# Performance work log

Measured on AMD Instinct MI355X. Metric: run time of the kernel, lower is better.

The kernel has to match this reference:

```python
import jax, jax.numpy as jnp
import numpy as np

B, S, I, H = 1024, 200, 4, 128  # batch, seq_len, interest_num, hidden_size
ROUTING_TIMES = 3
EPS = 1e-9


def setup_inputs() -> dict:
    key = jax.random.key(0)
    k1, k2, k3 = jax.random.split(key, 3)
    item_eb = jax.random.normal(k1, (B, S, H), dtype=jnp.float32)
    mask = jax.random.randint(k2, (B, S), 0, 2, dtype=jnp.int32)
    w = jax.random.normal(k3, (1, S, I * H, H), dtype=jnp.float32)
    return {"item_eb": item_eb, "mask": mask, "w": w}


def _squash_factor(cap):
    # cap: [B, I, 1, H]; standard capsule squash scale
    n = jnp.sum(jnp.square(cap), axis=-1, keepdims=True)
    return n / (1.0 + n) / jnp.sqrt(n + EPS)


def reference(item_eb, mask, w):
    # bilinear_type == 2: item_eb_hat[b,s,i] = sum_h w[0,s,i,h] * item_eb[b,s,h]
    hat = jnp.einsum('bsh,sjh->bsj', item_eb, w[0])          # [B, S, I*H]
    hat = hat.reshape(B, S, I, H).transpose(0, 2, 1, 3)      # [B, I, S, H]
    hat_iter = jax.lax.stop_gradient(hat)                    # stop_grad=True

    atten_mask = mask[:, None, :]                            # [B, 1, S] broadcasts over I
    capsule_weight = jnp.zeros((B, I, S), dtype=item_eb.dtype)

    interest_capsule = None
    for i in range(ROUTING_TIMES):
        sw = jax.nn.softmax(capsule_weight, axis=-1)         # [B, I, S]
        sw = jnp.where(atten_mask == 0, jnp.zeros_like(sw), sw)
        sw = sw[:, :, None, :]                               # [B, I, 1, S]
        src = hat_iter if i < ROUTING_TIMES - 1 else hat
        interest_capsule = jnp.matmul(sw, src)               # [B, I, 1, H]
        interest_capsule = _squash_factor(interest_capsule) * interest_capsule
        if i < ROUTING_TIMES - 1:
            # delta[b,i,s] = <hat_iter[b,i,s,:], capsule[b,i,0,:]>
            delta = jnp.matmul(hat_iter, jnp.swapaxes(interest_capsule, 2, 3))
            capsule_weight = capsule_weight + delta.reshape(B, I, S)

    return interest_capsule.reshape(B, I, H)
```

## Files before the change

### kernel.cpp

```cpp
#include <hip/hip_runtime.h>
#include <hip/hip_bf16.h>
#include <cstdint>

#define SDIM 200
#define HDIM 128
#define IDIM 4
#define BDIM 1024
#define LDK 72
#define LDEF 132

typedef __attribute__((ext_vector_type(8))) short short8;
typedef __attribute__((ext_vector_type(4))) float f32x4;

__device__ __forceinline__ ushort f32_to_bf16u(float f) {
    uint32_t u = __builtin_bit_cast(uint32_t, f);
    u += 0x7FFFu + ((u >> 16) & 1u);
    return (ushort)(u >> 16);
}
__device__ __forceinline__ float bf16u_to_f32(ushort h) {
    uint32_t u = ((uint32_t)h) << 16;
    return __builtin_bit_cast(float, u);
}
__device__ __forceinline__ void split8(const float* p, uint4* hi, uint4* lo) {
    union { ushort u[8]; uint4 v; } xh, xl;
    #pragma unroll
    for (int j = 0; j < 8; ++j) {
        float f = p[j];
        ushort h = f32_to_bf16u(f);
        float r = f - bf16u_to_f32(h);
        xh.u[j] = h;
        xl.u[j] = f32_to_bf16u(r);
    }
    *hi = xh.v; *lo = xl.v;
}

__global__ __launch_bounds__(256, 2) void hat_gemm(const float* __restrict__ item,
                                                   const float* __restrict__ w,
                                                   float* __restrict__ hat,
                                                   int b0, int nbt) {
    __shared__ ushort lds[4 * 128 * LDK];
    ushort* Wh0 = lds;
    ushort* Wl0 = lds + 128 * LDK;
    ushort* Wh1 = lds + 2 * 128 * LDK;
    ushort* Wl1 = lds + 3 * 128 * LDK;
    float*  ef  = (float*)lds;

    const int blk = blockIdx.x;
    const int bt = blk / SDIM;
    const int s  = blk % SDIM;
    const int t  = threadIdx.x;

    const int wave = t >> 6, lane = t & 63;
    const int wm = wave >> 1, wn = wave & 1;
    const int m0 = lane & 15, q = lane >> 4;

    short8 ah[2][2][4], al[2][2][4];
    {
        const float* ib = item +
            ((size_t)(b0 + bt * 128 + wm * 64 + m0) * SDIM + s) * HDIM;
        #pragma unroll
        for (int tm = 0; tm < 4; ++tm) {
            const float* p = ib + (size_t)(tm * 16) * SDIM * HDIM;
            #pragma unroll
            for (int st = 0; st < 2; ++st)
                #pragma unroll
                for (int kk = 0; kk < 2; ++kk) {
                    uint4 hi, lo;
                    split8(p + st * 64 + kk * 32 + q * 8, &hi, &lo);
                    ah[st][kk][tm] = __builtin_bit_cast(short8, hi);
                    al[st][kk][tm] = __builtin_bit_cast(short8, lo);
                }
        }
    }

    const float* wRow = w + (size_t)s * (IDIM * HDIM) * HDIM;

    #pragma unroll 1
    for (int ii = 0; ii < IDIM; ++ii) {
        if (ii) __syncthreads();
        const float* wB = wRow + (size_t)ii * HDIM * HDIM;

        #pragma unroll
        for (int c = t; c < 2048; c += 256) {
            int row = c >> 4, g = c & 15;
            int st = g >> 3, go = g & 7;
            uint4 hi, lo;
            split8(wB + (size_t)row * HDIM + st * 64 + go * 8, &hi, &lo);
            ushort* WH = st ? Wh1 : Wh0;
            ushort* WL = st ? Wl1 : Wl0;
            *(uint4*)(&WH[row * LDK + go * 8]) = hi;
            *(uint4*)(&WL[row * LDK + go * 8]) = lo;
        }
        __syncthreads();

        f32x4 acc[4][4];
        #pragma unroll
        for (int tm = 0; tm < 4; ++tm)
            #pragma unroll
            for (int tn = 0; tn < 4; ++tn)
                acc[tm][tn] = (f32x4){0.f, 0.f, 0.f, 0.f};

        #pragma unroll
        for (int st = 0; st < 2; ++st) {
            const ushort* WH = st ? Wh1 : Wh0;
            const ushort* WL = st ? Wl1 : Wl0;
            #pragma unroll
            for (int kk = 0; kk < 2; ++kk) {
                const int kof = kk * 32 + q * 8;
                short8 bh[4], bl[4];
                #pragma unroll
                for (int tn = 0; tn < 4; ++tn) {
                    int ro = (wn * 64 + tn * 16 + m0) * LDK + kof;
                    bh[tn] = *(const short8*)(&WH[ro]);
                    bl[tn] = *(const short8*)(&WL[ro]);
                }
                #pragma unroll
                for (int tm = 0; tm < 4; ++tm)
                    #pragma unroll
                    for (int tn = 0; tn < 4; ++tn) {
                        acc[tm][tn] = __builtin_amdgcn_mfma_f32_16x16x32_bf16(
                            ah[st][kk][tm], bl[tn], acc[tm][tn], 0, 0, 0);
                        acc[tm][tn] = __builtin_amdgcn_mfma_f32_16x16x32_bf16(
                            al[st][kk][tm], bh[tn], acc[tm][tn], 0, 0, 0);
                        acc[tm][tn] = __builtin_amdgcn_mfma_f32_16x16x32_bf16(
                            ah[st][kk][tm], bh[tn], acc[tm][tn], 0, 0, 0);
                    }
            }
        }
        __syncthreads();

        #pragma unroll
        for (int tm = 0; tm < 4; ++tm) {
            #pragma unroll
            for (int tn = 0; tn < 4; ++tn) {
                int col = wn * 64 + tn * 16 + m0;
                #pragma unroll
                for (int rg = 0; rg < 4; ++rg) {
                    int row = wm * 64 + tm * 16 + q * 4 + rg;
                    ef[row * LDEF + col] = acc[tm][tn][rg];
                }
            }
        }
        __syncthreads();
        #pragma unroll
        for (int c = t; c < 4096; c += 256) {
            int row = c >> 5, cc = c & 31;
            int bl_ = bt * 128 + row;
            float4 v = *(const float4*)(&ef[row * LDEF + cc * 4]);
            *(float4*)(hat + (((size_t)bl_ * IDIM + ii) * SDIM + s) * HDIM + cc * 4) = v;
        }
    }
}

__global__ __launch_bounds__(256, 3) void routing4(const float* __restrict__ hat,
                                                   const int* __restrict__ mask,
                                                   float* __restrict__ out, int b0) {
    __shared__ float cw[SDIM];
    __shared__ float eall[SDIM];
    __shared__ float ew[SDIM];
    __shared__ float icp[8 * HDIM];
    __shared__ float ic[HDIM];
    __shared__ float icf[HDIM];
    __shared__ int   mk[SDIM];

    const int blk = blockIdx.x;
    const int bl = blk >> 2, ii = blk & 3;
    const int b = b0 + bl;
    const int t = threadIdx.x, lane = t & 63, wv = t >> 6;
    const int hq = (t & 31) * 4;
    const int sg = t >> 5;
    const float* base = hat + ((size_t)bl * IDIM + ii) * (SDIM * HDIM);

    if (t < SDIM) mk[t] = mask[(size_t)b * SDIM + t];

    float4 pf[25];
    #pragma unroll
    for (int j = 0; j < 25; ++j)
        pf[j] = *(const float4*)(base + (size_t)(sg + 8 * j) * HDIM + hq);
    __syncthreads();

    {
        float4 u = {0.f, 0.f, 0.f, 0.f};
        #pragma unroll
        for (int j = 0; j < 25; ++j) {
            if (mk[sg + 8 * j]) {
                u.x += pf[j].x; u.y += pf[j].y; u.z += pf[j].z; u.w += pf[j].w;
            }
        }
        *(float4*)(&icp[sg * HDIM + hq]) = u;
    }
    __syncthreads();
    if (t < HDIM) {
        float v = 0.f;
        #pragma unroll
        for (int g = 0; g < 8; ++g) v += icp[g * HDIM + t];
        ic[t] = v * (1.0f / 200.0f);
    }
    __syncthreads();
    if (wv == 0) {
        float i0 = ic[lane], i1 = ic[lane + 64];
        float p = i0 * i0 + i1 * i1;
        #pragma unroll
        for (int off = 32; off > 0; off >>= 1) p += __shfl_xor(p, off);
        float fac = p / (1.0f + p) / sqrtf(p + 1e-9f);
        icf[lane] = i0 * fac;
        icf[lane + 64] = i1 * fac;
    }
    __syncthreads();

    for (int iter = 1; iter <= 2; ++iter) {
        float4 c4 = *(const float4*)(&icf[hq]);
        #pragma unroll
        for (int j = 0; j < 25; ++j) {
            float d = fmaf(pf[j].x, c4.x, fmaf(pf[j].y, c4.y,
                      fmaf(pf[j].z, c4.z, pf[j].w * c4.w)));
            d += __shfl_xor(d, 16);
            d += __shfl_xor(d, 8);
            d += __shfl_xor(d, 4);
            d += __shfl_xor(d, 2);
            d += __shfl_xor(d, 1);
            if ((t & 31) == 0) {
                int s = sg + 8 * j;
                cw[s] = (iter == 1) ? d : cw[s] + d;
            }
        }
        __syncthreads();

        float m = fmaxf(cw[lane], fmaxf(cw[lane + 64], cw[lane + 128]));
        if (lane < SDIM - 192) m = fmaxf(m, cw[lane + 192]);
        #pragma unroll
        for (int off = 32; off > 0; off >>= 1) m = fmaxf(m, __shfl_xor(m, off));
        if (t < SDIM) {
            float e = __expf(cw[t] - m);
            eall[t] = e;
            ew[t] = mk[t] ? e : 0.0f;
        }
        __syncthreads();

        float D = eall[lane] + eall[lane + 64] + eall[lane + 128]
                + ((lane < SDIM - 192) ? eall[lane + 192] : 0.0f);
        #pragma unroll
        for (int off = 32; off > 0; off >>= 1) D += __shfl_xor(D, off);

        {
            float4 u = {0.f, 0.f, 0.f, 0.f};
            #pragma unroll
            for (int j = 0; j < 25; ++j) {
                float wgt = ew[sg + 8 * j];
                u.x = fmaf(wgt, pf[j].x, u.x);
                u.y = fmaf(wgt, pf[j].y, u.y);
                u.z = fmaf(wgt, pf[j].z, u.z);
                u.w = fmaf(wgt, pf[j].w, u.w);
            }
            *(float4*)(&icp[sg * HDIM + hq]) = u;
        }
        __syncthreads();

        if (t < HDIM) {
            float v = 0.f;
            #pragma unroll
            for (int g = 0; g < 8; ++g) v += icp[g * HDIM + t];
            ic[t] = v / D;
        }
        __syncthreads();

        if (wv == 0) {
            float i0 = ic[lane], i1 = ic[lane + 64];
            float p = i0 * i0 + i1 * i1;
            #pragma unroll
            for (int off = 32; off > 0; off >>= 1) p += __shfl_xor(p, off);
            float fac = p / (1.0f + p) / sqrtf(p + 1e-9f);
            if (iter == 1) {
                icf[lane] = i0 * fac;
                icf[lane + 64] = i1 * fac;
            } else {
                out[((size_t)b * IDIM + ii) * HDIM + lane]      = i0 * fac;
                out[((size_t)b * IDIM + ii) * HDIM + lane + 64] = i1 * fac;
            }
        }
        if (iter == 1) __syncthreads();
    }
}

extern "C" void kernel_launch(void* const* d_in, const int* in_sizes, int n_in,
                              void* d_out, int out_size, void* d_ws, size_t ws_size,
                              hipStream_t stream) {
    const float* item = nullptr;
    const int*   msk  = nullptr;
    const float* w    = nullptr;
    for (int i = 0; i < n_in; ++i) {
        if (in_sizes[i] == BDIM * SDIM * HDIM)             item = (const float*)d_in[i];
        else if (in_sizes[i] == BDIM * SDIM)               msk  = (const int*)d_in[i];
        else if (in_sizes[i] == SDIM * IDIM * HDIM * HDIM) w    = (const float*)d_in[i];
    }
    if (!item) item = (const float*)d_in[0];
    if (!msk)  msk  = (const int*)d_in[1];
    if (!w)    w    = (const float*)d_in[2];

    float* hat = (float*)d_ws;
    float* out = (float*)d_out;

    const size_t perB = (size_t)IDIM * SDIM * HDIM * sizeof(float);
    size_t hatCap = ws_size / perB;
    int chunk = 512;
    if (hatCap < (size_t)chunk) chunk = (int)((hatCap / 128) * 128);
    if (chunk < 128) chunk = 128;
    for (int bb = 0; bb < BDIM; bb += chunk) {
        int cb = (BDIM - bb < chunk) ? (BDIM - bb) : chunk;
        int nbt = cb / 128;
        hat_gemm<<<nbt * SDIM, 256, 0, stream>>>(item, w, hat, bb, nbt);
        routing4<<<cb * IDIM, 256, 0, stream>>>(hat, msk, out, bb);
    }
}
```

Baseline: 529.0 us.

## Cut register and LDS footprint in hat GEMM and widen routing blocks

The hat GEMM stops keeping the whole split-bf16 item tile in registers and re-splits it per k-step. It halves LDS by staging W one 64-wide k-slab at a time and writes the epilogue in two halves, which allows three blocks per CU instead of two. The routing kernel moves to 512 threads, so each thread holds 13 prefetched rows instead of 25, which lowers register pressure and spreads the latency over more warps. In exchange the GEMM issues more global loads, repeats the bf16 split work and adds extra barriers.

```diff
diff --git a/kernel.cpp b/kernel.cpp
--- a/kernel.cpp
+++ b/kernel.cpp
@@ -34,16 +34,14 @@
     *hi = xh.v; *lo = xl.v;
 }
 
-__global__ __launch_bounds__(256, 2) void hat_gemm(const float* __restrict__ item,
+__global__ __launch_bounds__(256, 3) void hat_gemm(const float* __restrict__ item,
                                                    const float* __restrict__ w,
                                                    float* __restrict__ hat,
                                                    int b0, int nbt) {
-    __shared__ ushort lds[4 * 128 * LDK];
-    ushort* Wh0 = lds;
-    ushort* Wl0 = lds + 128 * LDK;
-    ushort* Wh1 = lds + 2 * 128 * LDK;
-    ushort* Wl1 = lds + 3 * 128 * LDK;
-    float*  ef  = (float*)lds;
+    __shared__ ushort lds[2 * 128 * LDK];
+    ushort* Wh = lds;
+    ushort* Wl = lds + 128 * LDK;
+    float*  ef = (float*)lds;
 
     const int blk = blockIdx.x;
     const int bt = blk / SDIM;
@@ -54,44 +52,13 @@
     const int wm = wave >> 1, wn = wave & 1;
     const int m0 = lane & 15, q = lane >> 4;
 
-    short8 ah[2][2][4], al[2][2][4];
-    {
-        const float* ib = item +
-            ((size_t)(b0 + bt * 128 + wm * 64 + m0) * SDIM + s) * HDIM;
-        #pragma unroll
-        for (int tm = 0; tm < 4; ++tm) {
-            const float* p = ib + (size_t)(tm * 16) * SDIM * HDIM;
-            #pragma unroll
-            for (int st = 0; st < 2; ++st)
-                #pragma unroll
-                for (int kk = 0; kk < 2; ++kk) {
-                    uint4 hi, lo;
-                    split8(p + st * 64 + kk * 32 + q * 8, &hi, &lo);
-                    ah[st][kk][tm] = __builtin_bit_cast(short8, hi);
-                    al[st][kk][tm] = __builtin_bit_cast(short8, lo);
-                }
-        }
-    }
-
+    const float* ib = item +
+        ((size_t)(b0 + bt * 128 + wm * 64 + m0) * SDIM + s) * HDIM;
     const float* wRow = w + (size_t)s * (IDIM * HDIM) * HDIM;
 
     #pragma unroll 1
     for (int ii = 0; ii < IDIM; ++ii) {
-        if (ii) __syncthreads();
         const float* wB = wRow + (size_t)ii * HDIM * HDIM;
-
-        #pragma unroll
-        for (int c = t; c < 2048; c += 256) {
-            int row = c >> 4, g = c & 15;
-            int st = g >> 3, go = g & 7;
-            uint4 hi, lo;
-            split8(wB + (size_t)row * HDIM + st * 64 + go * 8, &hi, &lo);
-            ushort* WH = st ? Wh1 : Wh0;
-            ushort* WL = st ? Wl1 : Wl0;
-            *(uint4*)(&WH[row * LDK + go * 8]) = hi;
-            *(uint4*)(&WL[row * LDK + go * 8]) = lo;
-        }
-        __syncthreads();
 
         f32x4 acc[4][4];
         #pragma unroll
@@ -102,63 +69,87 @@
 
         #pragma unroll
         for (int st = 0; st < 2; ++st) {
-            const ushort* WH = st ? Wh1 : Wh0;
-            const ushort* WL = st ? Wl1 : Wl0;
+            __syncthreads();
+
+            #pragma unroll
+            for (int c = t; c < 1024; c += 256) {
+                int row = c >> 3, g = c & 7;
+                uint4 hi, lo;
+                split8(wB + (size_t)row * HDIM + st * 64 + g * 8, &hi, &lo);
+                *(uint4*)(&Wh[row * LDK + g * 8]) = hi;
+                *(uint4*)(&Wl[row * LDK + g * 8]) = lo;
+            }
+            __syncthreads();
+
             #pragma unroll
             for (int kk = 0; kk < 2; ++kk) {
                 const int kof = kk * 32 + q * 8;
+                short8 a_h[4], a_l[4];
+                #pragma unroll
+                for (int tm = 0; tm < 4; ++tm) {
+                    uint4 hi, lo;
+                    split8(ib + (size_t)(tm * 16) * (SDIM * HDIM) + st * 64 + kof,
+                           &hi, &lo);
+                    a_h[tm] = __builtin_bit_cast(short8, hi);
+                    a_l[tm] = __builtin_bit_cast(short8, lo);
+                }
                 short8 bh[4], bl[4];
                 #pragma unroll
                 for (int tn = 0; tn < 4; ++tn) {
                     int ro = (wn * 64 + tn * 16 + m0) * LDK + kof;
-                    bh[tn] = *(const short8*)(&WH[ro]);
-                    bl[tn] = *(const short8*)(&WL[ro]);
+                    bh[tn] = *(const short8*)(&Wh[ro]);
+                    bl[tn] = *(const short8*)(&Wl[ro]);
                 }
                 #pragma unroll
                 for (int tm = 0; tm < 4; ++tm)
                     #pragma unroll
                     for (int tn = 0; tn < 4; ++tn) {
                         acc[tm][tn] = __builtin_amdgcn_mfma_f32_16x16x32_bf16(
-                            ah[st][kk][tm], bl[tn], acc[tm][tn], 0, 0, 0);
+                            a_h[tm], bl[tn], acc[tm][tn], 0, 0, 0);
                         acc[tm][tn] = __builtin_amdgcn_mfma_f32_16x16x32_bf16(
-                            al[st][kk][tm], bh[tn], acc[tm][tn], 0, 0, 0);
+                            a_l[tm], bh[tn], acc[tm][tn], 0, 0, 0);
                         acc[tm][tn] = __builtin_amdgcn_mfma_f32_16x16x32_bf16(
-                            ah[st][kk][tm], bh[tn], acc[tm][tn], 0, 0, 0);
+                            a_h[tm], bh[tn], acc[tm][tn], 0, 0, 0);
                     }
             }
         }
-        __syncthreads();
-
-        #pragma unroll
-        for (int tm = 0; tm < 4; ++tm) {
-            #pragma unroll
-            for (int tn = 0; tn < 4; ++tn) {
-                int col = wn * 64 + tn * 16 + m0;
+
+        #pragma unroll
+        for (int eh = 0; eh < 2; ++eh) {
+            __syncthreads();
+            if (wm == eh) {
                 #pragma unroll
-                for (int rg = 0; rg < 4; ++rg) {
-                    int row = wm * 64 + tm * 16 + q * 4 + rg;
-                    ef[row * LDEF + col] = acc[tm][tn][rg];
+                for (int tm = 0; tm < 4; ++tm) {
+                    #pragma unroll
+                    for (int tn = 0; tn < 4; ++tn) {
+                        int col = wn * 64 + tn * 16 + m0;
+                        #pragma unroll
+                        for (int rg = 0; rg < 4; ++rg) {
+                            int row = tm * 16 + q * 4 + rg;
+                            ef[row * LDEF + col] = acc[tm][tn][rg];
+                        }
+                    }
                 }
             }
-        }
-        __syncthreads();
-        #pragma unroll
-        for (int c = t; c < 4096; c += 256) {
-            int row = c >> 5, cc = c & 31;
-            int bl_ = bt * 128 + row;
-            float4 v = *(const float4*)(&ef[row * LDEF + cc * 4]);
-            *(float4*)(hat + (((size_t)bl_ * IDIM + ii) * SDIM + s) * HDIM + cc * 4) = v;
-        }
-    }
-}
-
-__global__ __launch_bounds__(256, 3) void routing4(const float* __restrict__ hat,
-                                                   const int* __restrict__ mask,
-                                                   float* __restrict__ out, int b0) {
+            __syncthreads();
+            #pragma unroll
+            for (int c = t; c < 2048; c += 256) {
+                int row = c >> 5, cc = c & 31;
+                int bl_ = bt * 128 + eh * 64 + row;
+                float4 v = *(const float4*)(&ef[row * LDEF + cc * 4]);
+                *(float4*)(hat + (((size_t)bl_ * IDIM + ii) * SDIM + s) * HDIM + cc * 4) = v;
+            }
+        }
+    }
+}
+
+__global__ __launch_bounds__(512) void routing4(const float* __restrict__ hat,
+                                                const int* __restrict__ mask,
+                                                float* __restrict__ out, int b0) {
     __shared__ float cw[SDIM];
     __shared__ float eall[SDIM];
     __shared__ float ew[SDIM];
-    __shared__ float icp[8 * HDIM];
+    __shared__ float icp[16 * HDIM];
     __shared__ float ic[HDIM];
     __shared__ float icf[HDIM];
     __shared__ int   mk[SDIM];
@@ -169,23 +160,29 @@
     const int t = threadIdx.x, lane = t & 63, wv = t >> 6;
     const int hq = (t & 31) * 4;
     const int sg = t >> 5;
+    const bool has13 = (sg < 8);
     const float* base = hat + ((size_t)bl * IDIM + ii) * (SDIM * HDIM);
 
     if (t < SDIM) mk[t] = mask[(size_t)b * SDIM + t];
 
-    float4 pf[25];
+    float4 pf[13];
     #pragma unroll
-    for (int j = 0; j < 25; ++j)
-        pf[j] = *(const float4*)(base + (size_t)(sg + 8 * j) * HDIM + hq);
+    for (int j = 0; j < 12; ++j)
+        pf[j] = *(const float4*)(base + (size_t)(sg + 16 * j) * HDIM + hq);
+    pf[12] = has13 ? *(const float4*)(base + (size_t)(sg + 192) * HDIM + hq)
+                   : (float4){0.f, 0.f, 0.f, 0.f};
     __syncthreads();
 
     {
         float4 u = {0.f, 0.f, 0.f, 0.f};
         #pragma unroll
-        for (int j = 0; j < 25; ++j) {
-            if (mk[sg + 8 * j]) {
+        for (int j = 0; j < 12; ++j) {
+            if (mk[sg + 16 * j]) {
                 u.x += pf[j].x; u.y += pf[j].y; u.z += pf[j].z; u.w += pf[j].w;
             }
+        }
+        if (has13 && mk[sg + 192]) {
+            u.x += pf[12].x; u.y += pf[12].y; u.z += pf[12].z; u.w += pf[12].w;
         }
         *(float4*)(&icp[sg * HDIM + hq]) = u;
     }
@@ -193,7 +190,7 @@
     if (t < HDIM) {
         float v = 0.f;
         #pragma unroll
-        for (int g = 0; g < 8; ++g) v += icp[g * HDIM + t];
+        for (int g = 0; g < 16; ++g) v += icp[g * HDIM + t];
         ic[t] = v * (1.0f / 200.0f);
     }
     __syncthreads();
@@ -211,7 +208,7 @@
     for (int iter = 1; iter <= 2; ++iter) {
         float4 c4 = *(const float4*)(&icf[hq]);
         #pragma unroll
-        for (int j = 0; j < 25; ++j) {
+        for (int j = 0; j < 13; ++j) {
             float d = fmaf(pf[j].x, c4.x, fmaf(pf[j].y, c4.y,
                       fmaf(pf[j].z, c4.z, pf[j].w * c4.w)));
             d += __shfl_xor(d, 16);
@@ -219,8 +216,8 @@
             d += __shfl_xor(d, 4);
             d += __shfl_xor(d, 2);
             d += __shfl_xor(d, 1);
-            if ((t & 31) == 0) {
-                int s = sg + 8 * j;
+            if ((t & 31) == 0 && (j < 12 || has13)) {
+                int s = sg + 16 * j;
                 cw[s] = (iter == 1) ? d : cw[s] + d;
             }
         }
@@ -245,13 +242,18 @@
         {
             float4 u = {0.f, 0.f, 0.f, 0.f};
             #pragma unroll
-            for (int j = 0; j < 25; ++j) {
-                float wgt = ew[sg + 8 * j];
+            for (int j = 0; j < 12; ++j) {
+                float wgt = ew[sg + 16 * j];
                 u.x = fmaf(wgt, pf[j].x, u.x);
                 u.y = fmaf(wgt, pf[j].y, u.y);
                 u.z = fmaf(wgt, pf[j].z, u.z);
                 u.w = fmaf(wgt, pf[j].w, u.w);
             }
+            float wgt = has13 ? ew[sg + 192] : 0.0f;
+            u.x = fmaf(wgt, pf[12].x, u.x);
+            u.y = fmaf(wgt, pf[12].y, u.y);
+            u.z = fmaf(wgt, pf[12].z, u.z);
+            u.w = fmaf(wgt, pf[12].w, u.w);
             *(float4*)(&icp[sg * HDIM + hq]) = u;
         }
         __syncthreads();
@@ -259,7 +261,7 @@
         if (t < HDIM) {
             float v = 0.f;
             #pragma unroll
-            for (int g = 0; g < 8; ++g) v += icp[g * HDIM + t];
+            for (int g = 0; g < 16; ++g) v += icp[g * HDIM + t];
             ic[t] = v / D;
         }
         __syncthreads();
@@ -309,6 +311,6 @@
         int cb = (BDIM - bb < chunk) ? (BDIM - bb) : chunk;
         int nbt = cb / 128;
         hat_gemm<<<nbt * SDIM, 256, 0, stream>>>(item, w, hat, bb, nbt);
-        routing4<<<cb * IDIM, 256, 0, stream>>>(hat, msk, out, bb);
-    }
-}
+        routing4<<<cb * IDIM, 512, 0, stream>>>(hat, msk, out, bb);
+    }
+}
```

Result: slower. 768.0 us (+45.2%).
